# Optimization experiments

Measured on AMD Instinct MI355X. Metric: run time of the kernel, lower is better.

The kernel has to match this reference:

```python
import jax, jax.numpy as jnp
import numpy as np

R_MAX = 5.0          # MACE default cutoff
P_CUT = 6            # polynomial cutoff exponent
AVG_NEIGH = 16.0     # MACE avg_num_neighbors normalization


def _sph_harm(u):
    """Real spherical harmonics l=0..3, e3nn 'component' normalization. u: [E,3] unit vectors -> [E,16]."""
    x, y, z = u[..., 0], u[..., 1], u[..., 2]
    s3, s5, s15 = np.sqrt(3.0), np.sqrt(5.0), np.sqrt(15.0)
    s35_8, s105, s21_8, s7 = np.sqrt(35.0 / 8.0), np.sqrt(105.0), np.sqrt(21.0 / 8.0), np.sqrt(7.0)
    one = jnp.ones_like(x)
    Y = [
        one,
        s3 * x, s3 * y, s3 * z,
        s15 * x * y, s15 * y * z, 0.5 * s5 * (3.0 * z * z - 1.0), s15 * x * z, 0.5 * s15 * (x * x - y * y),
        s35_8 * y * (3.0 * x * x - y * y), s105 * x * y * z, s21_8 * y * (5.0 * z * z - 1.0),
        0.5 * s7 * (5.0 * z * z * z - 3.0 * z), s21_8 * x * (5.0 * z * z - 1.0),
        0.5 * s105 * z * (x * x - y * y), s35_8 * x * (x * x - 3.0 * y * y),
    ]
    return jnp.stack(Y, axis=-1)


def _radial_embedding(r):
    """Bessel basis (8) times polynomial cutoff. r: [E] -> [E,8]."""
    n = jnp.arange(1, 9, dtype=r.dtype)
    rb = np.sqrt(2.0 / R_MAX) * jnp.sin(n * jnp.pi * r[:, None] / R_MAX) / r[:, None]
    uu = jnp.clip(r / R_MAX, 0.0, 1.0)
    p = float(P_CUT)
    f = (1.0 - 0.5 * (p + 1.0) * (p + 2.0) * uu ** p
         + p * (p + 2.0) * uu ** (p + 1.0)
         - 0.5 * p * (p + 1.0) * uu ** (p + 2.0))
    return rb * f[:, None]


def _forward(positions, shifts, node_attrs, W_embed, W_up, W_r1, W_r2, W_lin, W_skip, W_prod, Wcg, Wcg2, edge_index):
    N = positions.shape[0]
    snd, rcv = edge_index[0], edge_index[1]
    vec = positions[rcv] - positions[snd] + shifts            # [E,3]
    r = jnp.sqrt(jnp.maximum(jnp.sum(vec * vec, -1), 1e-12))  # [E]
    u = vec / r[:, None]
    edge_attrs = _sph_harm(u)                                 # [E,16]
    edge_feats = _radial_embedding(r)                         # [E,8]
    L = edge_attrs.shape[-1]
    k = W_embed.shape[1]
    # node embedding: scalars in the l=0 slot
    feats = jnp.zeros((N, k, L), positions.dtype).at[:, :, 0].set(node_attrs @ W_embed)
    invariants = []
    for i in range(W_up.shape[0]):
        up = jnp.einsum('nkL,kc->ncL', feats, W_up[i])                      # linear_up
        Rw = jax.nn.silu(edge_feats @ W_r1[i]) @ W_r2[i]                    # radial MLP [E,k]
        gathered = up[snd] * Rw[:, :, None]                                 # [E,k,16]
        # equivariant tensor product (coupling tensor plays the CG role)
        msg = jnp.einsum('eka,es,ast->ekt', gathered, edge_attrs, Wcg)      # [E,k,16]
        agg = jax.ops.segment_sum(msg, rcv, num_segments=N) / AVG_NEIGH     # scatter-sum
        mid = jnp.einsum('nkL,kc->ncL', agg, W_lin[i])
        # residual skip tensor product with species attrs
        sc = jnp.einsum('nkL,nz,zkc->ncL', feats, node_attrs, W_skip[i])
        # product block: symmetric (quadratic) contraction + linear + skip
        quad = jnp.einsum('nka,nkb,abt->nkt', mid, mid, Wcg2)
        feats = jnp.einsum('nkL,kc->ncL', mid + quad, W_prod[i]) + sc
        invariants.append(feats[:, :, 0])                                   # l=0 invariant slice [N,k]
    return jnp.concatenate(invariants, axis=-1)                             # [N, n_layers*k]


def setup_inputs() -> dict:
    key = jax.random.key(0)
    ks = jax.random.split(key, 12)
    N, E, Z, k, L, NB, H, NL = 8000, 128000, 10, 32, 16, 8, 32, 2
    positions = jax.random.normal(ks[0], (N, 3), dtype=jnp.float32) * 2.0
    edge_index = jax.random.randint(ks[1], (2, E), 0, N, dtype=jnp.int32)
    shifts = jnp.zeros((E, 3), jnp.float32)
    species = jax.random.randint(ks[2], (N,), 0, Z)
    node_attrs = jax.nn.one_hot(species, Z, dtype=jnp.float32)
    W_embed = jax.random.normal(ks[3], (Z, k), dtype=jnp.float32) / np.sqrt(Z)
    W_up = jax.random.normal(ks[4], (NL, k, k), dtype=jnp.float32) / np.sqrt(k)
    W_r1 = jax.random.normal(ks[5], (NL, NB, H), dtype=jnp.float32) / np.sqrt(NB)
    W_r2 = jax.random.normal(ks[6], (NL, H, k), dtype=jnp.float32) / np.sqrt(H)
    W_lin = jax.random.normal(ks[7], (NL, k, k), dtype=jnp.float32) / np.sqrt(k)
    W_skip = jax.random.normal(ks[8], (NL, Z, k, k), dtype=jnp.float32) / np.sqrt(Z * k)
    W_prod = jax.random.normal(ks[9], (NL, k, k), dtype=jnp.float32) / np.sqrt(k)
    Wcg = jax.random.normal(ks[10], (L, L, L), dtype=jnp.float32) * 0.1
    Wcg2 = jax.random.normal(ks[11], (L, L, L), dtype=jnp.float32) * 0.05
    return dict(positions=positions, shifts=shifts, node_attrs=node_attrs, W_embed=W_embed,
                W_up=W_up, W_r1=W_r1, W_r2=W_r2, W_lin=W_lin, W_skip=W_skip, W_prod=W_prod,
                Wcg=Wcg, Wcg2=Wcg2, edge_index=edge_index)


def reference(positions, shifts, node_attrs, W_embed, W_up, W_r1, W_r2, W_lin, W_skip, W_prod, Wcg, Wcg2, edge_index):
    return _forward(positions, shifts, node_attrs, W_embed, W_up, W_r1, W_r2, W_lin, W_skip, W_prod, Wcg, Wcg2, edge_index)
```

## Files before the change

kernel.cpp:

```cpp
#include <hip/hip_runtime.h>
#include <math.h>
#include <stdint.h>

#define N_NODES 8000
#define N_EDGES 128000
#define NZ 10
#define K 32
#define LDIM 16
#define NB 8
#define NH 32
#define NL 2

typedef _Float16 half8 __attribute__((ext_vector_type(8)));
typedef __attribute__((ext_vector_type(4))) float f32x4;

#define WAVE_SYNC() do { \
    asm volatile("s_waitcnt lgkmcnt(0)" ::: "memory"); \
    __builtin_amdgcn_wave_barrier(); \
    __builtin_amdgcn_sched_barrier(0); \
} while (0)

__global__ __launch_bounds__(256) void k_count(const int* __restrict__ ei,
                                               int* __restrict__ counts) {
    int e = blockIdx.x * 256 + threadIdx.x;
    if (e >= N_EDGES) return;
    atomicAdd(&counts[ei[N_EDGES + e]], 1);
}

__global__ __launch_bounds__(1024) void k_scan(const int* __restrict__ counts,
                                               int* __restrict__ row_ptr,
                                               int* __restrict__ woff) {
    __shared__ int s[8192];
    int tid = threadIdx.x;
    for (int j = tid; j < 8192; j += 1024) s[j] = (j < N_NODES) ? counts[j] : 0;
    __syncthreads();
    for (int off = 1; off < 8192; off <<= 1) {
        int v[8];
#pragma unroll
        for (int jj = 0; jj < 8; jj++) {
            int idx = tid + jj*1024;
            v[jj] = s[idx] + ((idx >= off) ? s[idx - off] : 0);
        }
        __syncthreads();
#pragma unroll
        for (int jj = 0; jj < 8; jj++) s[tid + jj*1024] = v[jj];
        __syncthreads();
    }
    for (int j = tid; j <= N_NODES; j += 1024) {
        int v = (j == 0) ? 0 : s[j-1];
        row_ptr[j] = v;
        if (j < N_NODES) woff[j] = v;
    }
}

__global__ __launch_bounds__(256) void k_scatter(const int* __restrict__ ei,
                                                 int* __restrict__ woff,
                                                 int* __restrict__ inv,
                                                 int* __restrict__ snd_csr) {
    int e = blockIdx.x * 256 + threadIdx.x;
    if (e >= N_EDGES) return;
    int r = ei[N_EDGES + e];
    int s = ei[e];
    int pp = atomicAdd(&woff[r], 1);
    inv[e] = pp;
    snd_csr[pp] = s;
}

__global__ __launch_bounds__(256) void k_geom(const float* __restrict__ pos,
                                              const float* __restrict__ shifts,
                                              const int* __restrict__ ei,
                                              const int* __restrict__ inv,
                                              float* __restrict__ Yc,
                                              float* __restrict__ efc) {
    int e = blockIdx.x * blockDim.x + threadIdx.x;
    if (e >= N_EDGES) return;
    int snd = ei[e];
    int rcv = ei[N_EDGES + e];
    int slot = inv[e];
    float vx = pos[rcv*3+0] - pos[snd*3+0] + shifts[e*3+0];
    float vy = pos[rcv*3+1] - pos[snd*3+1] + shifts[e*3+1];
    float vz = pos[rcv*3+2] - pos[snd*3+2] + shifts[e*3+2];
    float r2 = vx*vx + vy*vy + vz*vz;
    float r  = sqrtf(fmaxf(r2, 1e-12f));
    float inv_r = 1.0f / r;
    float x = vx*inv_r, y = vy*inv_r, z = vz*inv_r;

    const float s3    = 1.7320508075688772f;
    const float s5    = 2.2360679774997896f;
    const float s15   = 3.8729833462074170f;
    const float s35_8 = 2.0916500663351885f;
    const float s105  = 10.246950765959598f;
    const float s21_8 = 1.6201851746019651f;
    const float s7    = 2.6457513110645907f;

    float Yv[16];
    Yv[0]  = 1.0f;
    Yv[1]  = s3*x;  Yv[2] = s3*y;  Yv[3] = s3*z;
    Yv[4]  = s15*x*y;
    Yv[5]  = s15*y*z;
    Yv[6]  = 0.5f*s5*(3.0f*z*z - 1.0f);
    Yv[7]  = s15*x*z;
    Yv[8]  = 0.5f*s15*(x*x - y*y);
    Yv[9]  = s35_8*y*(3.0f*x*x - y*y);
    Yv[10] = s105*x*y*z;
    Yv[11] = s21_8*y*(5.0f*z*z - 1.0f);
    Yv[12] = 0.5f*s7*(5.0f*z*z*z - 3.0f*z);
    Yv[13] = s21_8*x*(5.0f*z*z - 1.0f);
    Yv[14] = 0.5f*s105*z*(x*x - y*y);
    Yv[15] = s35_8*x*(x*x - 3.0f*y*y);
#pragma unroll
    for (int j = 0; j < 16; j++) Yc[(size_t)slot*16 + j] = Yv[j];

    float uu = fminf(fmaxf(r * 0.2f, 0.0f), 1.0f);
    float u2 = uu*uu;
    float u6 = u2*u2*u2;
    float f  = 1.0f - 28.0f*u6 + 48.0f*u6*uu - 21.0f*u6*u2;
    float c  = 0.632455532033676f * inv_r * f;
    const float PI5 = 3.14159265358979323846f * 0.2f;
#pragma unroll
    for (int n = 1; n <= 8; n++) efc[(size_t)slot*8 + n - 1] = c * sinf((float)n * PI5 * r);
}

__global__ __launch_bounds__(256) void k_ww(const float* __restrict__ We,
                                            const float* __restrict__ Wup0,
                                            float* __restrict__ WW) {
    int i = blockIdx.x * 256 + threadIdx.x;
    if (i >= NZ * K) return;
    int z = i >> 5, c = i & 31;
    float a = 0.0f;
#pragma unroll
    for (int k = 0; k < K; ++k) a += We[z*K + k] * Wup0[k*K + c];
    WW[i] = a;
}

__global__ __launch_bounds__(256) void k_embed(const float* __restrict__ attrs,
                                               const float* __restrict__ We,
                                               const float* __restrict__ WW,
                                               float* __restrict__ feats,
                                               float* __restrict__ up0c,
                                               int* __restrict__ spec) {
    int i = blockIdx.x * blockDim.x + threadIdx.x;
    if (i >= N_NODES * K) return;
    int n = i >> 5, k = i & 31;
    float a = 0.0f, b = 0.0f;
#pragma unroll
    for (int z = 0; z < NZ; z++) {
        float av = attrs[n*NZ + z];
        a += av * We[z*K + k];
        b += av * WW[z*K + k];
    }
    float* f = feats + (size_t)n*(K*LDIM) + k*LDIM;
    f[0] = a;
#pragma unroll
    for (int j = 1; j < LDIM; j++) f[j] = 0.0f;
    up0c[(size_t)n*K + k] = b;
    if (k == 0) {
        int sp = 0; float best = -1.0f;
        for (int z = 0; z < NZ; z++) { float v = attrs[n*NZ + z]; if (v > best) { best = v; sp = z; } }
        spec[n] = sp;
    }
}

__global__ __launch_bounds__(256) void k_radial(const float* __restrict__ efc,
                                                const float* __restrict__ W1,
                                                const float* __restrict__ W2,
                                                float* __restrict__ Rwc) {
    __shared__ __align__(16) float lW1[NB*NH];
    __shared__ __align__(16) float lW2[NH*K];
    int tid = threadIdx.x;
    for (int j = tid; j < NB*NH; j += 256) lW1[j] = W1[j];
    for (int j = tid; j < NH*K;  j += 256) lW2[j] = W2[j];
    __syncthreads();
    int e = blockIdx.x * 256 + tid;
    if (e >= N_EDGES) return;
    const float4* e4 = (const float4*)(efc + (size_t)e*8);
    float4 ea = e4[0], eb = e4[1];
    float efr[8] = {ea.x, ea.y, ea.z, ea.w, eb.x, eb.y, eb.z, eb.w};
    float rw[32];
#pragma unroll
    for (int k = 0; k < 32; ++k) rw[k] = 0.0f;
    for (int j = 0; j < NH; ++j) {
        float h = 0.0f;
#pragma unroll
        for (int b = 0; b < NB; ++b) h += efr[b] * lW1[b*NH + j];
        float s = h / (1.0f + expf(-h));
        const float4* w2r = (const float4*)(lW2 + j*K);
#pragma unroll
        for (int kq = 0; kq < 8; ++kq) {
            float4 w = w2r[kq];
            rw[kq*4+0] += s*w.x; rw[kq*4+1] += s*w.y;
            rw[kq*4+2] += s*w.z; rw[kq*4+3] += s*w.w;
        }
    }
    float4* o = (float4*)(Rwc + (size_t)e*32);
#pragma unroll
    for (int kq = 0; kq < 8; ++kq)
        o[kq] = make_float4(rw[kq*4], rw[kq*4+1], rw[kq*4+2], rw[kq*4+3]);
}

__global__ __launch_bounds__(256, 3) void k_agg0(const float* __restrict__ up0c,
                                                 const float* __restrict__ Yc,
                                                 const float* __restrict__ Rwc,
                                                 const int* __restrict__ snd_csr,
                                                 const int* __restrict__ row_ptr,
                                                 const float* __restrict__ Wcg,
                                                 float* __restrict__ agg) {
    int tid = threadIdx.x;
    int wave = tid >> 6, lane = tid & 63;
    int n = blockIdx.x * 4 + wave;
    int k0 = lane & 15, tq = lane >> 4;

    float w0[16][4];
#pragma unroll
    for (int s = 0; s < 16; ++s) {
        float4 w = *(const float4*)(Wcg + s*16 + tq*4);
        w0[s][0]=w.x; w0[s][1]=w.y; w0[s][2]=w.z; w0[s][3]=w.w;
    }

    int start = row_ptr[n], end = row_ptr[n+1];
    float4 acc0 = {0,0,0,0}, acc1 = {0,0,0,0};

    if (start < end) {
        int snd = snd_csr[start];
        const float4* Yp = (const float4*)(Yc + (size_t)start*16);
        float4 y0=Yp[0], y1=Yp[1], y2=Yp[2], y3=Yp[3];
        float rw0 = Rwc[(size_t)start*32 + k0];
        float rw1 = Rwc[(size_t)start*32 + 16 + k0];
        float u0 = up0c[(size_t)snd*32 + k0];
        float u1 = up0c[(size_t)snd*32 + 16 + k0];

        for (int ii = start; ii < end; ++ii) {
            int ip = (ii + 1 < end) ? ii + 1 : ii;
            int nsnd = snd_csr[ip];
            const float4* Yn = (const float4*)(Yc + (size_t)ip*16);
            float4 ny0=Yn[0], ny1=Yn[1], ny2=Yn[2], ny3=Yn[3];
            float nrw0 = Rwc[(size_t)ip*32 + k0];
            float nrw1 = Rwc[(size_t)ip*32 + 16 + k0];
            float nu0 = up0c[(size_t)nsnd*32 + k0];
            float nu1 = up0c[(size_t)nsnd*32 + 16 + k0];

            float yv[16] = {y0.x,y0.y,y0.z,y0.w, y1.x,y1.y,y1.z,y1.w,
                            y2.x,y2.y,y2.z,y2.w, y3.x,y3.y,y3.z,y3.w};
            float c0=0.f, c1=0.f, c2=0.f, c3=0.f;
#pragma unroll
            for (int s = 0; s < 16; ++s) {
                c0 += yv[s]*w0[s][0]; c1 += yv[s]*w0[s][1];
                c2 += yv[s]*w0[s][2]; c3 += yv[s]*w0[s][3];
            }
            float g0 = rw0 * u0, g1 = rw1 * u1;
            acc0.x += g0*c0; acc0.y += g0*c1; acc0.z += g0*c2; acc0.w += g0*c3;
            acc1.x += g1*c0; acc1.y += g1*c1; acc1.z += g1*c2; acc1.w += g1*c3;

            y0=ny0; y1=ny1; y2=ny2; y3=ny3;
            rw0=nrw0; rw1=nrw1; u0=nu0; u1=nu1;
        }
    }

    float* ag = agg + (size_t)n*512;
    *(float4*)(ag + k0*16 + tq*4)        = make_float4(acc0.x*0.0625f, acc0.y*0.0625f,
                                                       acc0.z*0.0625f, acc0.w*0.0625f);
    *(float4*)(ag + (16+k0)*16 + tq*4)   = make_float4(acc1.x*0.0625f, acc1.y*0.0625f,
                                                       acc1.z*0.0625f, acc1.w*0.0625f);
}

__global__ __launch_bounds__(256, 2) void k_agg(const _Float16* __restrict__ up,
                                                const float* __restrict__ Yc,
                                                const float* __restrict__ Rwc,
                                                const int* __restrict__ snd_csr,
                                                const int* __restrict__ row_ptr,
                                                const float* __restrict__ Wcg,
                                                float* __restrict__ agg) {
    int tid = threadIdx.x;
    int wave = tid >> 6, lane = tid & 63;
    int n = blockIdx.x * 4 + wave;
    int t0 = lane & 15;
    int g  = lane >> 4;
    int h  = g & 1;
    int eo = g >> 1;

    float wr[8][16];
#pragma unroll
    for (int j = 0; j < 8; ++j)
#pragma unroll
        for (int s = 0; s < 16; ++s)
            wr[j][s] = Wcg[(8*h + j)*256 + s*16 + t0];

    int start = row_ptr[n], end = row_ptr[n+1];
    f32x4 accL = {0.f,0.f,0.f,0.f}, accH = {0.f,0.f,0.f,0.f};

    if (start < end) {
        int i0 = start + eo;     bool v0 = i0 < end; int q0 = v0 ? i0 : start;
        int i1 = i0 + 2;         bool v1 = i1 < end; int q1 = v1 ? i1 : start;
        int i2 = i0 + 4;         bool v2 = i2 < end; int q2 = v2 ? i2 : start;
        int snd0 = snd_csr[q0], snd1 = snd_csr[q1];
        int snd2 = snd_csr[q2];

        const float4* Y4 = (const float4*)(Yc + (size_t)q0*16);
        float4 y0=Y4[0], y1=Y4[1], y2=Y4[2], y3=Y4[3];
        float rwL = v0 ? Rwc[(size_t)q0*32 + t0]      : 0.0f;
        float rwH = v0 ? Rwc[(size_t)q0*32 + 16 + t0] : 0.0f;
        half8 u0L = *(const half8*)(up + (size_t)snd0*512 + t0*16 + 8*h);
        half8 u0H = *(const half8*)(up + (size_t)snd0*512 + (16+t0)*16 + 8*h);
        half8 u1L = *(const half8*)(up + (size_t)snd1*512 + t0*16 + 8*h);
        half8 u1H = *(const half8*)(up + (size_t)snd1*512 + (16+t0)*16 + 8*h);

        int npair = (end - start + 1) >> 1;
        for (int p = 0; p < npair; ++p) {
            half8 u2L = *(const half8*)(up + (size_t)snd2*512 + t0*16 + 8*h);
            half8 u2H = *(const half8*)(up + (size_t)snd2*512 + (16+t0)*16 + 8*h);
            int in1 = start + 2*(p+1) + eo; bool vn1 = in1 < end; int qn1 = vn1 ? in1 : start;
            const float4* nY = (const float4*)(Yc + (size_t)qn1*16);
            float4 ny0=nY[0], ny1=nY[1], ny2=nY[2], ny3=nY[3];
            float nrwL = vn1 ? Rwc[(size_t)qn1*32 + t0]      : 0.0f;
            float nrwH = vn1 ? Rwc[(size_t)qn1*32 + 16 + t0] : 0.0f;
            int in3 = start + 2*(p+3) + eo; bool vn3 = in3 < end; int qn3 = vn3 ? in3 : start;
            int snd3 = snd_csr[qn3];

            float yv[16] = {y0.x,y0.y,y0.z,y0.w, y1.x,y1.y,y1.z,y1.w,
                            y2.x,y2.y,y2.z,y2.w, y3.x,y3.y,y3.z,y3.w};
            float c[8] = {0,0,0,0,0,0,0,0};
#pragma unroll
            for (int s = 0; s < 16; ++s) {
#pragma unroll
                for (int j = 0; j < 8; ++j) c[j] += yv[s]*wr[j][s];
            }

            half8 bf, rvL, rvH;
            _Float16 rwLh = (_Float16)rwL, rwHh = (_Float16)rwH;
#pragma unroll
            for (int j = 0; j < 8; ++j) { bf[j] = (_Float16)c[j]; rvL[j] = rwLh; rvH[j] = rwHh; }
            half8 afL = u0L * rvL;
            half8 afH = u0H * rvH;

            accL = __builtin_amdgcn_mfma_f32_16x16x32_f16(afL, bf, accL, 0, 0, 0);
            accH = __builtin_amdgcn_mfma_f32_16x16x32_f16(afH, bf, accH, 0, 0, 0);

            y0=ny0; y1=ny1; y2=ny2; y3=ny3;
            rwL=nrwL; rwH=nrwH;
            u0L=u1L; u0H=u1H; u1L=u2L; u1H=u2H;
            snd2 = snd3;
        }
    }

    float* ag = agg + (size_t)n*512;
#pragma unroll
    for (int e = 0; e < 4; ++e) {
        ag[(4*g + e)*16 + t0]      = accL[e] * 0.0625f;
        ag[(16 + 4*g + e)*16 + t0] = accH[e] * 0.0625f;
    }
}

__global__ __launch_bounds__(256, 2) void k_node(const float* __restrict__ agg,
                                                 float* __restrict__ feats,
                                                 const int* __restrict__ spec,
                                                 const float* __restrict__ Wlin,
                                                 const float* __restrict__ Wskip,
                                                 const float* __restrict__ Wprod,
                                                 const float* __restrict__ Wcg2,
                                                 float* __restrict__ out,
                                                 int layer,
                                                 const float* __restrict__ Wup_next,
                                                 _Float16* __restrict__ up_next,
                                                 int has_up) {
    __shared__ __align__(16) float lWsym[136*16];
    __shared__ __align__(16) float lWlin[1024];
    __shared__ __align__(16) float lWprod[1024];
    __shared__ __align__(16) float lWup[1024];
    __shared__ __align__(16) float lagg[4096];

    int tid = threadIdx.x;
    int nbase = blockIdx.x * 8;
    for (int j = tid; j < 136*16; j += 256) {
        int p = j >> 4, t = j & 15;
        int a = 0;
#pragma unroll
        for (int aa = 1; aa < 16; ++aa)
            if (p >= aa*16 - (aa*(aa-1))/2) a = aa;
        int b = a + (p - (a*16 - (a*(a-1))/2));
        float v = Wcg2[a*256 + b*16 + t];
        if (b > a) v += Wcg2[b*256 + a*16 + t];
        lWsym[j] = v;
    }
    for (int j = tid; j < 1024; j += 256) { lWlin[j] = Wlin[j]; lWprod[j] = Wprod[j]; }
    if (has_up) for (int j = tid; j < 1024; j += 256) lWup[j] = Wup_next[j];
    {
        const float4* src = (const float4*)(agg + (size_t)nbase*512);
        float4* dst = (float4*)lagg;
        for (int j = tid; j < 1024; j += 256) dst[j] = src[j];
    }
    __syncthreads();

    int lane = tid & 63;
    int wave = tid >> 6;
    int c = lane & 31;
    int node = wave*2 + (lane >> 5);
    int n = nbase + node;
    const float* la = lagg + node*512;

    float m[16];
#pragma unroll
    for (int t = 0; t < 16; ++t) m[t] = 0.0f;
    for (int k = 0; k < 32; ++k) {
        float w = lWlin[k*32 + c];
        const float4* ar = (const float4*)(la + k*16);
        float4 a0 = ar[0], a1 = ar[1], a2 = ar[2], a3 = ar[3];
        m[0]+=a0.x*w;  m[1]+=a0.y*w;  m[2]+=a0.z*w;  m[3]+=a0.w*w;
        m[4]+=a1.x*w;  m[5]+=a1.y*w;  m[6]+=a1.z*w;  m[7]+=a1.w*w;
        m[8]+=a2.x*w;  m[9]+=a2.y*w;  m[10]+=a2.z*w; m[11]+=a2.w*w;
        m[12]+=a3.x*w; m[13]+=a3.y*w; m[14]+=a3.z*w; m[15]+=a3.w*w;
    }

    float q[16];
#pragma unroll
    for (int t = 0; t < 16; ++t) q[t] = 0.0f;
    {
        int p = 0;
#pragma unroll
        for (int a = 0; a < 16; ++a) {
#pragma unroll
            for (int b = a; b < 16; ++b) {
                float pm = m[a] * m[b];
                const float4* w4 = (const float4*)(lWsym + p*16);
                float4 w0 = w4[0], w1 = w4[1], w2 = w4[2], w3 = w4[3];
                q[0]+=pm*w0.x;  q[1]+=pm*w0.y;  q[2]+=pm*w0.z;  q[3]+=pm*w0.w;
                q[4]+=pm*w1.x;  q[5]+=pm*w1.y;  q[6]+=pm*w1.z;  q[7]+=pm*w1.w;
                q[8]+=pm*w2.x;  q[9]+=pm*w2.y;  q[10]+=pm*w2.z; q[11]+=pm*w2.w;
                q[12]+=pm*w3.x; q[13]+=pm*w3.y; q[14]+=pm*w3.z; q[15]+=pm*w3.w;
                ++p;
            }
        }
    }

    float* lsrow = lagg + node*512 + c*16;
    WAVE_SYNC();
#pragma unroll
    for (int tq = 0; tq < 4; ++tq)
        *((float4*)(lsrow + tq*4)) = make_float4(m[tq*4]+q[tq*4], m[tq*4+1]+q[tq*4+1],
                                                 m[tq*4+2]+q[tq*4+2], m[tq*4+3]+q[tq*4+3]);
    WAVE_SYNC();

    int sp = spec[n];
    const float* wsk = Wskip + (size_t)sp*1024;
    const float* ls_node = lagg + node*512;
    const float* fg = feats + (size_t)n*512;
    float acc[16];
#pragma unroll
    for (int t = 0; t < 16; ++t) acc[t] = 0.0f;
    for (int k = 0; k < 32; ++k) {
        float wp = lWprod[k*32 + c];
        float wv = wsk[k*32 + c];
        const float4* sr = (const float4*)(ls_node + k*16);
        float4 s0 = sr[0], s1 = sr[1], s2 = sr[2], s3 = sr[3];
        const float4* fr = (const float4*)(fg + k*16);
        float4 f0 = fr[0], f1 = fr[1], f2 = fr[2], f3 = fr[3];
        acc[0]+=s0.x*wp+f0.x*wv;  acc[1]+=s0.y*wp+f0.y*wv;
        acc[2]+=s0.z*wp+f0.z*wv;  acc[3]+=s0.w*wp+f0.w*wv;
        acc[4]+=s1.x*wp+f1.x*wv;  acc[5]+=s1.y*wp+f1.y*wv;
        acc[6]+=s1.z*wp+f1.z*wv;  acc[7]+=s1.w*wp+f1.w*wv;
        acc[8]+=s2.x*wp+f2.x*wv;  acc[9]+=s2.y*wp+f2.y*wv;
        acc[10]+=s2.z*wp+f2.z*wv; acc[11]+=s2.w*wp+f2.w*wv;
        acc[12]+=s3.x*wp+f3.x*wv; acc[13]+=s3.y*wp+f3.y*wv;
        acc[14]+=s3.z*wp+f3.z*wv; acc[15]+=s3.w*wp+f3.w*wv;
    }
    out[(size_t)n*(NL*K) + layer*K + c] = acc[0];

    if (has_up) {
        float* fo = feats + (size_t)n*512 + c*16;
#pragma unroll
        for (int tq = 0; tq < 4; ++tq)
            *((float4*)(fo + tq*4)) = make_float4(acc[tq*4], acc[tq*4+1], acc[tq*4+2], acc[tq*4+3]);

        WAVE_SYNC();
        float* lfrow = lagg + node*512 + c*16;
#pragma unroll
        for (int tq = 0; tq < 4; ++tq)
            *((float4*)(lfrow + tq*4)) = make_float4(acc[tq*4], acc[tq*4+1], acc[tq*4+2], acc[tq*4+3]);
        WAVE_SYNC();

        float u[16];
#pragma unroll
        for (int t = 0; t < 16; ++t) u[t] = 0.0f;
        const float* lf_node = lagg + node*512;
        for (int k = 0; k < 32; ++k) {
            float w = lWup[k*32 + c];
            const float4* frr = (const float4*)(lf_node + k*16);
            float4 f0 = frr[0], f1 = frr[1], f2 = frr[2], f3 = frr[3];
            u[0]+=f0.x*w;  u[1]+=f0.y*w;  u[2]+=f0.z*w;  u[3]+=f0.w*w;
            u[4]+=f1.x*w;  u[5]+=f1.y*w;  u[6]+=f1.z*w;  u[7]+=f1.w*w;
            u[8]+=f2.x*w;  u[9]+=f2.y*w;  u[10]+=f2.z*w; u[11]+=f2.w*w;
            u[12]+=f3.x*w; u[13]+=f3.y*w; u[14]+=f3.z*w; u[15]+=f3.w*w;
        }
        half8 h0, h1;
#pragma unroll
        for (int j = 0; j < 8; ++j) { h0[j] = (_Float16)u[j]; h1[j] = (_Float16)u[8+j]; }
        _Float16* uo = up_next + (size_t)n*512 + c*16;
        *(half8*)(uo)     = h0;
        *(half8*)(uo + 8) = h1;
    }
}

extern "C" void kernel_launch(void* const* d_in, const int* in_sizes, int n_in,
                              void* d_out, int out_size, void* d_ws, size_t ws_size,
                              hipStream_t stream) {
    const float* pos     = (const float*)d_in[0];
    const float* shifts  = (const float*)d_in[1];
    const float* attrs   = (const float*)d_in[2];
    const float* W_embed = (const float*)d_in[3];
    const float* W_up    = (const float*)d_in[4];
    const float* W_r1    = (const float*)d_in[5];
    const float* W_r2    = (const float*)d_in[6];
    const float* W_lin   = (const float*)d_in[7];
    const float* W_skip  = (const float*)d_in[8];
    const float* W_prod  = (const float*)d_in[9];
    const float* Wcg     = (const float*)d_in[10];
    const float* Wcg2    = (const float*)d_in[11];
    const int*   ei      = (const int*)d_in[12];
    float* out = (float*)d_out;

    uint8_t* p = (uint8_t*)d_ws;
    auto alloc = [&](size_t bytes) -> void* {
        void* r = (void*)p;
        p += (bytes + 255) & ~size_t(255);
        return r;
    };
    float* Yc        = (float*)alloc((size_t)N_EDGES * 16 * sizeof(float));
    float* efc       = (float*)alloc((size_t)N_EDGES * 8  * sizeof(float));
    float* Rwc       = (float*)alloc((size_t)N_EDGES * K  * sizeof(float));
    float* feats     = (float*)alloc((size_t)N_NODES * K * LDIM * sizeof(float));
    _Float16* up_h   = (_Float16*)alloc((size_t)N_NODES * K * LDIM * sizeof(_Float16));
    float* agg       = (float*)alloc((size_t)N_NODES * K * LDIM * sizeof(float));
    float* up0c      = (float*)alloc((size_t)N_NODES * K * sizeof(float));
    float* WW        = (float*)alloc((size_t)NZ * K * sizeof(float));
    int* counts   = (int*)alloc((size_t)N_NODES * sizeof(int));
    int* woff     = (int*)alloc((size_t)N_NODES * sizeof(int));
    int* row_ptr  = (int*)alloc((size_t)(N_NODES + 1) * sizeof(int));
    int* inv      = (int*)alloc((size_t)N_EDGES * sizeof(int));
    int* snd_csr  = (int*)alloc((size_t)N_EDGES * sizeof(int));
    int* spec     = (int*)alloc((size_t)N_NODES * sizeof(int));

    hipMemsetAsync(counts, 0, N_NODES * sizeof(int), stream);
    k_count<<<(N_EDGES + 255) / 256, 256, 0, stream>>>(ei, counts);
    k_scan<<<1, 1024, 0, stream>>>(counts, row_ptr, woff);
    k_scatter<<<(N_EDGES + 255) / 256, 256, 0, stream>>>(ei, woff, inv, snd_csr);
    k_geom<<<(N_EDGES + 255) / 256, 256, 0, stream>>>(pos, shifts, ei, inv, Yc, efc);
    k_ww<<<2, 256, 0, stream>>>(W_embed, W_up, WW);
    k_embed<<<(N_NODES * K + 255) / 256, 256, 0, stream>>>(attrs, W_embed, WW, feats, up0c, spec);

    k_radial<<<(N_EDGES + 255) / 256, 256, 0, stream>>>(efc, W_r1, W_r2, Rwc);
    k_agg0<<<N_NODES/4, 256, 0, stream>>>(up0c, Yc, Rwc, snd_csr, row_ptr, Wcg, agg);
    k_node<<<N_NODES/8, 256, 0, stream>>>(agg, feats, spec, W_lin, W_skip, W_prod, Wcg2,
                                          out, 0, W_up + (size_t)1*K*K, up_h, 1);

    k_radial<<<(N_EDGES + 255) / 256, 256, 0, stream>>>(efc, W_r1 + (size_t)1*NB*NH,
                                                        W_r2 + (size_t)1*NH*K, Rwc);
    k_agg<<<N_NODES/4, 256, 0, stream>>>(up_h, Yc, Rwc, snd_csr, row_ptr, Wcg, agg);
    k_node<<<N_NODES/8, 256, 0, stream>>>(agg, feats, spec,
                                          W_lin + (size_t)1*K*K, W_skip + (size_t)1*NZ*K*K,
                                          W_prod + (size_t)1*K*K, Wcg2, out, 1,
                                          W_up, up_h, 0);
}
```

Baseline: 269.5 us.

## Precompute symmetric CG weights once and shrink k_node shared memory

Moves the symmetrized Wcg2 construction into a separate one-time kernel writing a global Wsym buffer, which k_node now reads directly instead of rebuilding it in LDS in every block. It drops the LDS staging of agg (reading it straight from global) and uses a smaller padded per-node scratch row (stride 20) for the intermediate products, raising launch bounds to 3 blocks per CU. The intent is to cut per-block setup work and LDS footprint to improve occupancy. The cost is that the quadratic Wsym reads and the agg reads now go through global/cache memory instead of LDS. An else branch is also added for the final layer.

```diff
diff --git a/kernel.cpp b/kernel.cpp
--- a/kernel.cpp
+++ b/kernel.cpp
@@ -133,6 +133,20 @@
     WW[i] = a;
 }
 
+__global__ __launch_bounds__(256) void k_wsym(const float* __restrict__ Wcg2,
+                                              float* __restrict__ Wsym) {
+    int j = blockIdx.x * 256 + threadIdx.x;
+    if (j >= 136*16) return;
+    int p = j >> 4, t = j & 15;
+    int a = 0;
+    for (int aa = 1; aa < 16; ++aa)
+        if (p >= aa*16 - (aa*(aa-1))/2) a = aa;
+    int b = a + (p - (a*16 - (a*(a-1))/2));
+    float v = Wcg2[a*256 + b*16 + t];
+    if (b > a) v += Wcg2[b*256 + a*16 + t];
+    Wsym[j] = v;
+}
+
 __global__ __launch_bounds__(256) void k_embed(const float* __restrict__ attrs,
                                                const float* __restrict__ We,
                                                const float* __restrict__ WW,
@@ -350,44 +364,28 @@
     }
 }
 
-__global__ __launch_bounds__(256, 2) void k_node(const float* __restrict__ agg,
+#define SROW 20
+__global__ __launch_bounds__(256, 3) void k_node(const float* __restrict__ agg,
                                                  float* __restrict__ feats,
                                                  const int* __restrict__ spec,
                                                  const float* __restrict__ Wlin,
                                                  const float* __restrict__ Wskip,
                                                  const float* __restrict__ Wprod,
-                                                 const float* __restrict__ Wcg2,
+                                                 const float* __restrict__ Wsym,
                                                  float* __restrict__ out,
                                                  int layer,
                                                  const float* __restrict__ Wup_next,
                                                  _Float16* __restrict__ up_next,
                                                  int has_up) {
-    __shared__ __align__(16) float lWsym[136*16];
     __shared__ __align__(16) float lWlin[1024];
     __shared__ __align__(16) float lWprod[1024];
     __shared__ __align__(16) float lWup[1024];
-    __shared__ __align__(16) float lagg[4096];
+    __shared__ __align__(16) float lS[8*32*SROW];
 
     int tid = threadIdx.x;
     int nbase = blockIdx.x * 8;
-    for (int j = tid; j < 136*16; j += 256) {
-        int p = j >> 4, t = j & 15;
-        int a = 0;
-#pragma unroll
-        for (int aa = 1; aa < 16; ++aa)
-            if (p >= aa*16 - (aa*(aa-1))/2) a = aa;
-        int b = a + (p - (a*16 - (a*(a-1))/2));
-        float v = Wcg2[a*256 + b*16 + t];
-        if (b > a) v += Wcg2[b*256 + a*16 + t];
-        lWsym[j] = v;
-    }
     for (int j = tid; j < 1024; j += 256) { lWlin[j] = Wlin[j]; lWprod[j] = Wprod[j]; }
     if (has_up) for (int j = tid; j < 1024; j += 256) lWup[j] = Wup_next[j];
-    {
-        const float4* src = (const float4*)(agg + (size_t)nbase*512);
-        float4* dst = (float4*)lagg;
-        for (int j = tid; j < 1024; j += 256) dst[j] = src[j];
-    }
     __syncthreads();
 
     int lane = tid & 63;
@@ -395,14 +393,14 @@
     int c = lane & 31;
     int node = wave*2 + (lane >> 5);
     int n = nbase + node;
-    const float* la = lagg + node*512;
+    const float* ga = agg + (size_t)n*512;
 
     float m[16];
 #pragma unroll
     for (int t = 0; t < 16; ++t) m[t] = 0.0f;
     for (int k = 0; k < 32; ++k) {
         float w = lWlin[k*32 + c];
-        const float4* ar = (const float4*)(la + k*16);
+        const float4* ar = (const float4*)(ga + k*16);
         float4 a0 = ar[0], a1 = ar[1], a2 = ar[2], a3 = ar[3];
         m[0]+=a0.x*w;  m[1]+=a0.y*w;  m[2]+=a0.z*w;  m[3]+=a0.w*w;
         m[4]+=a1.x*w;  m[5]+=a1.y*w;  m[6]+=a1.z*w;  m[7]+=a1.w*w;
@@ -420,7 +418,7 @@
 #pragma unroll
             for (int b = a; b < 16; ++b) {
                 float pm = m[a] * m[b];
-                const float4* w4 = (const float4*)(lWsym + p*16);
+                const float4* w4 = (const float4*)(Wsym + p*16);
                 float4 w0 = w4[0], w1 = w4[1], w2 = w4[2], w3 = w4[3];
                 q[0]+=pm*w0.x;  q[1]+=pm*w0.y;  q[2]+=pm*w0.z;  q[3]+=pm*w0.w;
                 q[4]+=pm*w1.x;  q[5]+=pm*w1.y;  q[6]+=pm*w1.z;  q[7]+=pm*w1.w;
@@ -431,8 +429,7 @@
         }
     }
 
-    float* lsrow = lagg + node*512 + c*16;
-    WAVE_SYNC();
+    float* lsrow = lS + (node*32 + c)*SROW;
 #pragma unroll
     for (int tq = 0; tq < 4; ++tq)
         *((float4*)(lsrow + tq*4)) = make_float4(m[tq*4]+q[tq*4], m[tq*4+1]+q[tq*4+1],
@@ -441,7 +438,6 @@
 
     int sp = spec[n];
     const float* wsk = Wskip + (size_t)sp*1024;
-    const float* ls_node = lagg + node*512;
     const float* fg = feats + (size_t)n*512;
     float acc[16];
 #pragma unroll
@@ -449,7 +445,7 @@
     for (int k = 0; k < 32; ++k) {
         float wp = lWprod[k*32 + c];
         float wv = wsk[k*32 + c];
-        const float4* sr = (const float4*)(ls_node + k*16);
+        const float4* sr = (const float4*)(lS + (node*32 + k)*SROW);
         float4 s0 = sr[0], s1 = sr[1], s2 = sr[2], s3 = sr[3];
         const float4* fr = (const float4*)(fg + k*16);
         float4 f0 = fr[0], f1 = fr[1], f2 = fr[2], f3 = fr[3];
@@ -471,19 +467,17 @@
             *((float4*)(fo + tq*4)) = make_float4(acc[tq*4], acc[tq*4+1], acc[tq*4+2], acc[tq*4+3]);
 
         WAVE_SYNC();
-        float* lfrow = lagg + node*512 + c*16;
 #pragma unroll
         for (int tq = 0; tq < 4; ++tq)
-            *((float4*)(lfrow + tq*4)) = make_float4(acc[tq*4], acc[tq*4+1], acc[tq*4+2], acc[tq*4+3]);
+            *((float4*)(lsrow + tq*4)) = make_float4(acc[tq*4], acc[tq*4+1], acc[tq*4+2], acc[tq*4+3]);
         WAVE_SYNC();
 
         float u[16];
 #pragma unroll
         for (int t = 0; t < 16; ++t) u[t] = 0.0f;
-        const float* lf_node = lagg + node*512;
         for (int k = 0; k < 32; ++k) {
             float w = lWup[k*32 + c];
-            const float4* frr = (const float4*)(lf_node + k*16);
+            const float4* frr = (const float4*)(lS + (node*32 + k)*SROW);
             float4 f0 = frr[0], f1 = frr[1], f2 = frr[2], f3 = frr[3];
             u[0]+=f0.x*w;  u[1]+=f0.y*w;  u[2]+=f0.z*w;  u[3]+=f0.w*w;
             u[4]+=f1.x*w;  u[5]+=f1.y*w;  u[6]+=f1.z*w;  u[7]+=f1.w*w;
@@ -496,6 +490,11 @@
         _Float16* uo = up_next + (size_t)n*512 + c*16;
         *(half8*)(uo)     = h0;
         *(half8*)(uo + 8) = h1;
+    } else {
+        float* fo = feats + (size_t)n*512 + c*16;
+#pragma unroll
+        for (int tq = 0; tq < 4; ++tq)
+            *((float4*)(fo + tq*4)) = make_float4(acc[tq*4], acc[tq*4+1], acc[tq*4+2], acc[tq*4+3]);
     }
 }
 
@@ -531,6 +530,7 @@
     float* agg       = (float*)alloc((size_t)N_NODES * K * LDIM * sizeof(float));
     float* up0c      = (float*)alloc((size_t)N_NODES * K * sizeof(float));
     float* WW        = (float*)alloc((size_t)NZ * K * sizeof(float));
+    float* Wsym      = (float*)alloc((size_t)136 * 16 * sizeof(float));
     int* counts   = (int*)alloc((size_t)N_NODES * sizeof(int));
     int* woff     = (int*)alloc((size_t)N_NODES * sizeof(int));
     int* row_ptr  = (int*)alloc((size_t)(N_NODES + 1) * sizeof(int));
@@ -544,11 +544,12 @@
     k_scatter<<<(N_EDGES + 255) / 256, 256, 0, stream>>>(ei, woff, inv, snd_csr);
     k_geom<<<(N_EDGES + 255) / 256, 256, 0, stream>>>(pos, shifts, ei, inv, Yc, efc);
     k_ww<<<2, 256, 0, stream>>>(W_embed, W_up, WW);
+    k_wsym<<<(136*16 + 255) / 256, 256, 0, stream>>>(Wcg2, Wsym);
     k_embed<<<(N_NODES * K + 255) / 256, 256, 0, stream>>>(attrs, W_embed, WW, feats, up0c, spec);
 
     k_radial<<<(N_EDGES + 255) / 256, 256, 0, stream>>>(efc, W_r1, W_r2, Rwc);
     k_agg0<<<N_NODES/4, 256, 0, stream>>>(up0c, Yc, Rwc, snd_csr, row_ptr, Wcg, agg);
-    k_node<<<N_NODES/8, 256, 0, stream>>>(agg, feats, spec, W_lin, W_skip, W_prod, Wcg2,
+    k_node<<<N_NODES/8, 256, 0, stream>>>(agg, feats, spec, W_lin, W_skip, W_prod, Wsym,
                                           out, 0, W_up + (size_t)1*K*K, up_h, 1);
 
     k_radial<<<(N_EDGES + 255) / 256, 256, 0, stream>>>(efc, W_r1 + (size_t)1*NB*NH,
@@ -556,6 +557,6 @@
     k_agg<<<N_NODES/4, 256, 0, stream>>>(up_h, Yc, Rwc, snd_csr, row_ptr, Wcg, agg);
     k_node<<<N_NODES/8, 256, 0, stream>>>(agg, feats, spec,
                                           W_lin + (size_t)1*K*K, W_skip + (size_t)1*NZ*K*K,
-                                          W_prod + (size_t)1*K*K, Wcg2, out, 1,
+                                          W_prod + (size_t)1*K*K, Wsym, out, 1,
                                           W_up, up_h, 0);
 }
```

After: 273.4 us. About the same (+1.4%).
